# Performance work log

Measured on AMD Instinct MI355X. Metric: run time of the kernel, lower is better.

The kernel has to match this reference:

```python
import jax, jax.numpy as jnp
import numpy as np

EPS_BN = 1e-5
EPS_NORM = 1e-12
USER_NUM, ITEM_NUM = 100000, 50000
N_NODES = USER_NUM + ITEM_NUM
N_EDGES = 2400000
OUT_DIM, HID_DIM = 64, 128
BATCH = 4096


def setup_inputs() -> dict:
    key = jax.random.key(0)
    ks = jax.random.split(key, 12)
    f32 = jnp.float32
    return {
        "user_emb": jax.random.normal(ks[0], (USER_NUM, OUT_DIM), f32) * 0.1,
        "item_emb": jax.random.normal(ks[1], (ITEM_NUM, OUT_DIM), f32) * 0.1,
        "W0": jax.random.normal(ks[2], (OUT_DIM, HID_DIM), f32) * (1.0 / np.sqrt(OUT_DIM)),
        "b0": jnp.zeros((HID_DIM,), f32),
        "g0": jnp.ones((HID_DIM,), f32),
        "beta0": jnp.zeros((HID_DIM,), f32),
        "W1": jax.random.normal(ks[3], (HID_DIM, HID_DIM), f32) * (1.0 / np.sqrt(HID_DIM)),
        "b1": jnp.zeros((HID_DIM,), f32),
        "g1": jnp.ones((HID_DIM,), f32),
        "beta1": jnp.zeros((HID_DIM,), f32),
        "W2": jax.random.normal(ks[4], (HID_DIM, OUT_DIM), f32) * (1.0 / np.sqrt(HID_DIM)),
        "b2": jnp.zeros((OUT_DIM,), f32),
        "user_id": jax.random.randint(ks[5], (BATCH,), 0, USER_NUM),
        "pos_item": jax.random.randint(ks[6], (BATCH,), 0, ITEM_NUM),
        "neg_item": jax.random.randint(ks[7], (BATCH,), 0, ITEM_NUM),
        "edge_index": jax.random.randint(ks[8], (2, N_EDGES), 0, N_NODES),
    }


def _gcn_conv(x, W, b, src, dst, dis):
    # GCNConv with self-loops and symmetric normalization:
    # out_i = sum_{j->i} d_j^{-1/2} d_i^{-1/2} (x_j W) + d_i^{-1} (x_i W) + b
    h = x @ W                                   # [N, F]
    norm = dis[src] * dis[dst]                  # [E]
    msgs = h[src] * norm[:, None]               # [E, F] (irregular gather)
    agg = jax.ops.segment_sum(msgs, dst, num_segments=x.shape[0])
    self_loop = h * (dis * dis)[:, None]        # contribution of added self-loops
    return agg + self_loop + b


def _bn_train(x, gamma, beta):
    mean = jnp.mean(x, axis=0)
    var = jnp.mean((x - mean) ** 2, axis=0)     # biased var, as torch BN uses
    return (x - mean) * jax.lax.rsqrt(var + EPS_BN) * gamma + beta


def _l2norm(x):
    n = jnp.sqrt(jnp.sum(x * x, axis=-1, keepdims=True))
    return x / jnp.maximum(n, EPS_NORM)


def reference(user_emb, item_emb, W0, b0, g0, beta0, W1, b1, g1, beta1, W2, b2,
              user_id, pos_item, neg_item, edge_index):
    N = user_emb.shape[0] + item_emb.shape[0]
    src, dst = edge_index[0], edge_index[1]
    # degree includes self loop (weight 1 per edge + 1 self loop)
    deg = 1.0 + jax.ops.segment_sum(jnp.ones_like(src, user_emb.dtype), dst, num_segments=N)
    dis = jax.lax.rsqrt(deg)

    x = jnp.concatenate([user_emb, item_emb], axis=0)          # [N, OUT_DIM]

    # layer 0: conv -> BN -> ReLU -> (dropout: eval/identity) -> L2-normalize
    x = _l2norm(jax.nn.relu(_bn_train(_gcn_conv(x, W0, b0, src, dst, dis), g0, beta0)))
    # layer 1
    x = _l2norm(jax.nn.relu(_bn_train(_gcn_conv(x, W1, b1, src, dst, dis), g1, beta1)))
    # final conv
    x = _gcn_conv(x, W2, b2, src, dst, dis)                    # [N, OUT_DIM]

    user_embeddings = x[:user_emb.shape[0]]
    item_embeddings = x[user_emb.shape[0]:]
    u = user_embeddings[user_id]
    p = item_embeddings[pos_item]
    n = item_embeddings[neg_item]
    pos_score = jnp.sum(u * p, axis=-1)
    neg_score = jnp.sum(u * n, axis=-1)
    rec_loss = -jnp.mean(jax.nn.log_sigmoid(pos_score - neg_score))
    return rec_loss, x
```

## Files before the change

kernel.cpp:

```cpp
#include <hip/hip_runtime.h>
#include <hip/hip_bf16.h>
#include <math.h>

#define USER_NUM 100000
#define ITEM_NUM 50000
#define N_NODES  150000
#define N_EDGES  2400000
#define OUT_DIM  64
#define HID_DIM  128
#define BATCH    4096
#define EPS_BN   1e-5f

typedef unsigned short ushort_t;
typedef unsigned int uint_t;

__device__ __forceinline__ ushort_t f2bf(float f) {
    uint_t u = __float_as_uint(f);
    u += 0x7FFFu + ((u >> 16) & 1u);
    return (ushort_t)(u >> 16);
}
__device__ __forceinline__ float bf2f(ushort_t s) {
    return __uint_as_float((uint_t)s << 16);
}


__global__ __launch_bounds__(256) void zero_int_kernel(int* __restrict__ p, int n) {
    int i = blockIdx.x * 256 + threadIdx.x;
    if (i < n) p[i] = 0;
}

__global__ __launch_bounds__(256) void count_kernel(const int* __restrict__ dst, int* __restrict__ cnt) {
    int i = blockIdx.x * 256 + threadIdx.x;
    if (i < N_EDGES) atomicAdd(&cnt[dst[i]], 1);
}

__global__ __launch_bounds__(256) void dis_kernel(const int* __restrict__ cnt, float* __restrict__ dis) {
    int i = blockIdx.x * 256 + threadIdx.x;
    if (i < N_NODES) dis[i] = rsqrtf(1.0f + (float)cnt[i]);
}

#define SC_ELEM 1024
#define SC_NB   ((N_NODES + SC_ELEM - 1) / SC_ELEM)

__global__ __launch_bounds__(256) void scan_part_kernel(const int* __restrict__ cnt,
                                                        int* __restrict__ psum) {
    __shared__ int red[4];
    int tid = threadIdx.x;
    int base = blockIdx.x * SC_ELEM + tid * 4;
    int s = 0;
#pragma unroll
    for (int j = 0; j < 4; j++) { int i = base + j; if (i < N_NODES) s += cnt[i]; }
#pragma unroll
    for (int d = 1; d < 64; d <<= 1) s += __shfl_xor(s, d);
    if ((tid & 63) == 0) red[tid >> 6] = s;
    __syncthreads();
    if (tid == 0) psum[blockIdx.x] = red[0] + red[1] + red[2] + red[3];
}

__global__ __launch_bounds__(256) void scan_mid_kernel(int* __restrict__ psum,
                                                       int* __restrict__ off, int nb) {
    __shared__ int lds[256];
    int tid = threadIdx.x;
    int v = (tid < nb) ? psum[tid] : 0;
    lds[tid] = v;
    __syncthreads();
    for (int d = 1; d < 256; d <<= 1) {
        int t = (tid >= d) ? lds[tid - d] : 0;
        __syncthreads();
        lds[tid] += t;
        __syncthreads();
    }
    if (tid < nb) psum[tid] = lds[tid] - v;
    if (tid == 0) off[N_NODES] = lds[255];
}

__global__ __launch_bounds__(256) void scan_emit_kernel(const int* __restrict__ cnt,
                                                        const int* __restrict__ psum,
                                                        int* __restrict__ off,
                                                        int* __restrict__ cur) {
    __shared__ int lds[256];
    int tid = threadIdx.x;
    int base = blockIdx.x * SC_ELEM + tid * 4;
    int v[4]; int s = 0;
#pragma unroll
    for (int j = 0; j < 4; j++) {
        int i = base + j;
        v[j] = (i < N_NODES) ? cnt[i] : 0;
        s += v[j];
    }
    lds[tid] = s;
    __syncthreads();
    for (int d = 1; d < 256; d <<= 1) {
        int t = (tid >= d) ? lds[tid - d] : 0;
        __syncthreads();
        lds[tid] += t;
        __syncthreads();
    }
    int run = psum[blockIdx.x] + lds[tid] - s;
#pragma unroll
    for (int j = 0; j < 4; j++) {
        int i = base + j;
        if (i < N_NODES) { off[i] = run; cur[i] = run; }
        run += v[j];
    }
}

__global__ __launch_bounds__(256) void fill_kernel(const int* __restrict__ src, const int* __restrict__ dst,
                                                   const float* __restrict__ dis,
                                                   int* __restrict__ cursor,
                                                   uint2* __restrict__ csr8) {
    int i = blockIdx.x * 256 + threadIdx.x;
    if (i < N_EDGES) {
        int s = src[i];
        int d = dst[i];
        int p = atomicAdd(&cursor[d], 1);
        uint2 e;
        e.x = (uint_t)s;
        e.y = __float_as_uint(dis[s] * dis[d]);
        csr8[p] = e;
    }
}


__device__ __forceinline__ float4 load4(const float* p) { return *(const float4*)p; }
__device__ __forceinline__ float4 load4(const ushort_t* p) {
    ushort4 u = *(const ushort4*)p;
    return make_float4(bf2f(u.x), bf2f(u.y), bf2f(u.z), bf2f(u.w));
}

template<typename XT, int DIN, int DOUT, int MBLK>
__global__ __launch_bounds__(256) void gemm_kernel(const XT* __restrict__ xlo,
                                                   const XT* __restrict__ xhi, int split,
                                                   const float* __restrict__ W,
                                                   ushort_t* __restrict__ out, int nrows) {
    constexpr int KC    = 32;
    constexpr int NC    = DIN / KC;
    constexpr int XS_PT = MBLK / 32;
    constexpr int WS_PT = DOUT / 32;
    constexpr int NCOLG = DOUT / 8;

    __shared__ float xs[MBLK][KC + 1];
    __shared__ float ws[KC][DOUT];

    const int tid  = threadIdx.x;
    const int row0 = blockIdx.x * MBLK;
    const int colg = tid % NCOLG;
    const int rowg = tid / NCOLG;

    float4 xr[XS_PT], wr[WS_PT];

    auto load_chunk = [&](int kc) {
#pragma unroll
        for (int i = 0; i < XS_PT; i++) {
            int idx = i * 256 + tid;
            int m = idx >> 3, kq = idx & 7;
            int row = row0 + m; if (row > nrows - 1) row = nrows - 1;
            const XT* rp = (row < split) ? xlo + (size_t)row * DIN
                                         : xhi + (size_t)(row - split) * DIN;
            xr[i] = load4(rp + kc + kq * 4);
        }
#pragma unroll
        for (int i = 0; i < WS_PT; i++) {
            int idx = i * 256 + tid;
            int n4 = idx % (DOUT / 4), kk = idx / (DOUT / 4);
            wr[i] = *(const float4*)(W + (size_t)(kc + kk) * DOUT + n4 * 4);
        }
    };
    auto write_chunk = [&]() {
#pragma unroll
        for (int i = 0; i < XS_PT; i++) {
            int idx = i * 256 + tid;
            int m = idx >> 3, kq = idx & 7;
            xs[m][kq * 4 + 0] = xr[i].x;
            xs[m][kq * 4 + 1] = xr[i].y;
            xs[m][kq * 4 + 2] = xr[i].z;
            xs[m][kq * 4 + 3] = xr[i].w;
        }
#pragma unroll
        for (int i = 0; i < WS_PT; i++) {
            int idx = i * 256 + tid;
            int n4 = idx % (DOUT / 4), kk = idx / (DOUT / 4);
            *(float4*)&ws[kk][n4 * 4] = wr[i];
        }
    };

    float acc[8][8];
#pragma unroll
    for (int r = 0; r < 8; r++)
#pragma unroll
        for (int c = 0; c < 8; c++) acc[r][c] = 0.f;

    load_chunk(0);
    write_chunk();
    __syncthreads();

    for (int c = 0; c < NC; c++) {
        if (c + 1 < NC) load_chunk((c + 1) * KC);
#pragma unroll 4
        for (int k = 0; k < KC; k++) {
            float4 wa = *(const float4*)&ws[k][colg * 8];
            float4 wb = *(const float4*)&ws[k][colg * 8 + 4];
            float xv[8];
#pragma unroll
            for (int r = 0; r < 8; r++) xv[r] = xs[rowg * 8 + r][k];
#pragma unroll
            for (int r = 0; r < 8; r++) {
                acc[r][0] = fmaf(xv[r], wa.x, acc[r][0]);
                acc[r][1] = fmaf(xv[r], wa.y, acc[r][1]);
                acc[r][2] = fmaf(xv[r], wa.z, acc[r][2]);
                acc[r][3] = fmaf(xv[r], wa.w, acc[r][3]);
                acc[r][4] = fmaf(xv[r], wb.x, acc[r][4]);
                acc[r][5] = fmaf(xv[r], wb.y, acc[r][5]);
                acc[r][6] = fmaf(xv[r], wb.z, acc[r][6]);
                acc[r][7] = fmaf(xv[r], wb.w, acc[r][7]);
            }
        }
        __syncthreads();
        if (c + 1 < NC) { write_chunk(); __syncthreads(); }
    }

#pragma unroll
    for (int r = 0; r < 8; r++) {
        int row = row0 + rowg * 8 + r;
        if (row < nrows) {
            uint4 pk;
            pk.x = (uint_t)f2bf(acc[r][0]) | ((uint_t)f2bf(acc[r][1]) << 16);
            pk.y = (uint_t)f2bf(acc[r][2]) | ((uint_t)f2bf(acc[r][3]) << 16);
            pk.z = (uint_t)f2bf(acc[r][4]) | ((uint_t)f2bf(acc[r][5]) << 16);
            pk.w = (uint_t)f2bf(acc[r][6]) | ((uint_t)f2bf(acc[r][7]) << 16);
            *(uint4*)&out[(size_t)row * DOUT + colg * 8] = pk;
        }
    }
}


template<int DOUT>
__global__ __launch_bounds__(256) void agg_kernel(const ushort_t* __restrict__ h,
                                                  const float* __restrict__ dis,
                                                  const int* __restrict__ off,
                                                  const uint2* __restrict__ csr8,
                                                  const float* __restrict__ bias,
                                                  float* __restrict__ out, int n) {
    int wave = threadIdx.x >> 6;
    int lane = threadIdx.x & 63;
    int node = blockIdx.x * 4 + wave;
    if (node >= n) return;
    float di  = dis[node];
    int   beg = off[node], end = off[node + 1];
    if (DOUT == 128) {
        const uint_t* hp = (const uint_t*)h;
        float ax = 0.f, ay = 0.f;
        int e = beg;
        for (; e + 4 <= end; e += 4) {
            uint2 e0 = csr8[e], e1 = csr8[e + 1], e2 = csr8[e + 2], e3 = csr8[e + 3];
            uint_t u0 = hp[(size_t)e0.x * 64 + lane];
            uint_t u1 = hp[(size_t)e1.x * 64 + lane];
            uint_t u2 = hp[(size_t)e2.x * 64 + lane];
            uint_t u3 = hp[(size_t)e3.x * 64 + lane];
            float w0 = __uint_as_float(e0.y), w1 = __uint_as_float(e1.y);
            float w2 = __uint_as_float(e2.y), w3 = __uint_as_float(e3.y);
            ax = fmaf(__uint_as_float(u0 << 16), w0, ax);
            ay = fmaf(__uint_as_float(u0 & 0xFFFF0000u), w0, ay);
            ax = fmaf(__uint_as_float(u1 << 16), w1, ax);
            ay = fmaf(__uint_as_float(u1 & 0xFFFF0000u), w1, ay);
            ax = fmaf(__uint_as_float(u2 << 16), w2, ax);
            ay = fmaf(__uint_as_float(u2 & 0xFFFF0000u), w2, ay);
            ax = fmaf(__uint_as_float(u3 << 16), w3, ax);
            ay = fmaf(__uint_as_float(u3 & 0xFFFF0000u), w3, ay);
        }
        for (; e < end; e++) {
            uint2 ev = csr8[e];
            float wv = __uint_as_float(ev.y);
            uint_t u = hp[(size_t)ev.x * 64 + lane];
            ax = fmaf(__uint_as_float(u << 16), wv, ax);
            ay = fmaf(__uint_as_float(u & 0xFFFF0000u), wv, ay);
        }
        uint_t us = hp[(size_t)node * 64 + lane];
        float2 bb = ((const float2*)bias)[lane];
        float dd = di * di;
        float2 o;
        o.x = ax + __uint_as_float(us << 16) * dd + bb.x;
        o.y = ay + __uint_as_float(us & 0xFFFF0000u) * dd + bb.y;
        ((float2*)out)[(size_t)node * 64 + lane] = o;
    } else {
        float ax = 0.f;
        int e = beg;
        for (; e + 4 <= end; e += 4) {
            uint2 e0 = csr8[e], e1 = csr8[e + 1], e2 = csr8[e + 2], e3 = csr8[e + 3];
            float h0 = bf2f(h[(size_t)e0.x * 64 + lane]);
            float h1 = bf2f(h[(size_t)e1.x * 64 + lane]);
            float h2 = bf2f(h[(size_t)e2.x * 64 + lane]);
            float h3 = bf2f(h[(size_t)e3.x * 64 + lane]);
            ax = fmaf(h0, __uint_as_float(e0.y), ax);
            ax = fmaf(h1, __uint_as_float(e1.y), ax);
            ax = fmaf(h2, __uint_as_float(e2.y), ax);
            ax = fmaf(h3, __uint_as_float(e3.y), ax);
        }
        for (; e < end; e++) {
            uint2 ev = csr8[e];
            ax = fmaf(bf2f(h[(size_t)ev.x * 64 + lane]), __uint_as_float(ev.y), ax);
        }
        float hs = bf2f(h[(size_t)node * 64 + lane]);
        out[(size_t)node * 64 + lane] = ax + hs * di * di + bias[lane];
    }
}


#define STATS_NB 512

__global__ __launch_bounds__(128) void stats1_kernel(const float* __restrict__ x,
                                                     double* __restrict__ part) {
    int col = threadIdx.x;
    double a = 0.0, b = 0.0;
    for (int row = blockIdx.x; row < N_NODES; row += STATS_NB) {
        float v = x[(size_t)row * HID_DIM + col];
        a += v;
        b += (double)v * (double)v;
    }
    part[(size_t)blockIdx.x * 256 + col]       = a;
    part[(size_t)blockIdx.x * 256 + 128 + col] = b;
}

__global__ __launch_bounds__(256) void stats2_kernel(const double* __restrict__ part,
                                                     const float* __restrict__ g,
                                                     const float* __restrict__ beta,
                                                     float* __restrict__ a_out,
                                                     float* __restrict__ b_out) {
    __shared__ double red1[4], red2[4];
    int col = blockIdx.x;
    int tid = threadIdx.x;
    double s1 = 0.0, s2 = 0.0;
    for (int p = tid; p < STATS_NB; p += 256) {
        s1 += part[(size_t)p * 256 + col];
        s2 += part[(size_t)p * 256 + 128 + col];
    }
#pragma unroll
    for (int d = 32; d >= 1; d >>= 1) {
        s1 += __shfl_xor(s1, d);
        s2 += __shfl_xor(s2, d);
    }
    int wave = tid >> 6, lane = tid & 63;
    if (lane == 0) { red1[wave] = s1; red2[wave] = s2; }
    __syncthreads();
    if (tid == 0) {
        double t1 = red1[0] + red1[1] + red1[2] + red1[3];
        double t2 = red2[0] + red2[1] + red2[2] + red2[3];
        double mean = t1 / (double)N_NODES;
        double var  = t2 / (double)N_NODES - mean * mean;
        float inv = rsqrtf((float)var + EPS_BN);
        float aa  = g[col] * inv;
        a_out[col] = aa;
        b_out[col] = beta[col] - (float)mean * aa;
    }
}


__global__ __launch_bounds__(256) void bn_relu_l2_kernel(const float* __restrict__ in,
                                                         const float* __restrict__ a,
                                                         const float* __restrict__ b,
                                                         uint_t* __restrict__ outp, int n) {
    int wave = threadIdx.x >> 6;
    int lane = threadIdx.x & 63;
    int row  = blockIdx.x * 4 + wave;
    if (row >= n) return;
    float2 v  = *(const float2*)(in + (size_t)row * 128 + lane * 2);
    float2 aa = *(const float2*)(a + lane * 2);
    float2 bb = *(const float2*)(b + lane * 2);
    float y0 = fmaxf(fmaf(v.x, aa.x, bb.x), 0.f);
    float y1 = fmaxf(fmaf(v.y, aa.y, bb.y), 0.f);
    float ss = y0 * y0 + y1 * y1;
#pragma unroll
    for (int d = 32; d >= 1; d >>= 1) ss += __shfl_xor(ss, d);
    float nn  = sqrtf(ss);
    float inv = 1.f / fmaxf(nn, 1e-12f);
    uint_t pk = (uint_t)f2bf(y0 * inv) | ((uint_t)f2bf(y1 * inv) << 16);
    outp[(size_t)row * 64 + lane] = pk;
}


__global__ void zero_float_kernel(float* p) { *p = 0.f; }

__global__ __launch_bounds__(256) void loss_kernel(const float* __restrict__ X,
                                                   const int* __restrict__ uid,
                                                   const int* __restrict__ pid,
                                                   const int* __restrict__ nid,
                                                   float* __restrict__ out0) {
    int wave = threadIdx.x >> 6;
    int lane = threadIdx.x & 63;
    int b = blockIdx.x * 4 + wave;
    if (b >= BATCH) return;
    const float* u = X + (size_t)uid[b] * OUT_DIM;
    const float* p = X + (size_t)(USER_NUM + pid[b]) * OUT_DIM;
    const float* q = X + (size_t)(USER_NUM + nid[b]) * OUT_DIM;
    float uv = u[lane];
    float ps = uv * p[lane];
    float ns = uv * q[lane];
#pragma unroll
    for (int d = 32; d >= 1; d >>= 1) {
        ps += __shfl_xor(ps, d);
        ns += __shfl_xor(ns, d);
    }
    if (lane == 0) {
        float t  = ns - ps;
        float sp = fmaxf(t, 0.f) + log1pf(expf(-fabsf(t)));
        atomicAdd(out0, sp * (1.0f / BATCH));
    }
}


extern "C" void kernel_launch(void* const* d_in, const int* in_sizes, int n_in,
                              void* d_out, int out_size, void* d_ws, size_t ws_size,
                              hipStream_t stream) {
    const float* user_emb = (const float*)d_in[0];
    const float* item_emb = (const float*)d_in[1];
    const float* W0  = (const float*)d_in[2];
    const float* b0  = (const float*)d_in[3];
    const float* g0  = (const float*)d_in[4];
    const float* be0 = (const float*)d_in[5];
    const float* W1  = (const float*)d_in[6];
    const float* b1  = (const float*)d_in[7];
    const float* g1  = (const float*)d_in[8];
    const float* be1 = (const float*)d_in[9];
    const float* W2  = (const float*)d_in[10];
    const float* b2  = (const float*)d_in[11];
    const int* user_id  = (const int*)d_in[12];
    const int* pos_item = (const int*)d_in[13];
    const int* neg_item = (const int*)d_in[14];
    const int* edge     = (const int*)d_in[15];
    const int* src = edge;
    const int* dst = edge + N_EDGES;

    char* w = (char*)d_ws;
    auto alloc = [&](size_t bytes) -> char* {
        char* r = w;
        w += (bytes + 255) / 256 * 256;
        return r;
    };
    int*      cnt  = (int*)alloc((size_t)N_NODES * 4);
    int*      off  = (int*)alloc((size_t)(N_NODES + 1) * 4);
    int*      cur  = (int*)alloc((size_t)N_NODES * 4);
    uint2*    csr8 = (uint2*)alloc((size_t)N_EDGES * 8);
    float*    dis  = (float*)alloc((size_t)N_NODES * 4);
    int*      psum = (int*)alloc((size_t)SC_NB * 4);
    double*   part = (double*)alloc((size_t)STATS_NB * 256 * 8);
    float*    bn_a = (float*)alloc(128 * 4);
    float*    bn_b = (float*)alloc(128 * 4);
    ushort_t* hbuf = (ushort_t*)alloc((size_t)N_NODES * HID_DIM * 2);
    float*    xbuf = (float*)alloc((size_t)N_NODES * HID_DIM * 4);
    ushort_t* xbf  = (ushort_t*)alloc((size_t)N_NODES * HID_DIM * 2);

    float* out = (float*)d_out;
    float* X   = out + 1;

    const int EB = (N_EDGES + 255) / 256;
    const int NB = (N_NODES + 255) / 256;
    const int AGGB = (N_NODES + 3) / 4;

    zero_int_kernel<<<NB, 256, 0, stream>>>(cnt, N_NODES);
    count_kernel<<<EB, 256, 0, stream>>>(dst, cnt);
    dis_kernel<<<NB, 256, 0, stream>>>(cnt, dis);
    scan_part_kernel<<<SC_NB, 256, 0, stream>>>(cnt, psum);
    scan_mid_kernel<<<1, 256, 0, stream>>>(psum, off, SC_NB);
    scan_emit_kernel<<<SC_NB, 256, 0, stream>>>(cnt, psum, off, cur);
    fill_kernel<<<EB, 256, 0, stream>>>(src, dst, dis, cur, csr8);

    gemm_kernel<float, 64, 128, 128><<<(N_NODES + 127) / 128, 256, 0, stream>>>(
        user_emb, item_emb, USER_NUM, W0, hbuf, N_NODES);
    agg_kernel<128><<<AGGB, 256, 0, stream>>>(hbuf, dis, off, csr8, b0, xbuf, N_NODES);
    stats1_kernel<<<STATS_NB, 128, 0, stream>>>(xbuf, part);
    stats2_kernel<<<128, 256, 0, stream>>>(part, g0, be0, bn_a, bn_b);
    bn_relu_l2_kernel<<<AGGB, 256, 0, stream>>>(xbuf, bn_a, bn_b, (uint_t*)xbf, N_NODES);

    gemm_kernel<ushort_t, 128, 128, 128><<<(N_NODES + 127) / 128, 256, 0, stream>>>(
        xbf, xbf, N_NODES, W1, hbuf, N_NODES);
    agg_kernel<128><<<AGGB, 256, 0, stream>>>(hbuf, dis, off, csr8, b1, xbuf, N_NODES);
    stats1_kernel<<<STATS_NB, 128, 0, stream>>>(xbuf, part);
    stats2_kernel<<<128, 256, 0, stream>>>(part, g1, be1, bn_a, bn_b);
    bn_relu_l2_kernel<<<AGGB, 256, 0, stream>>>(xbuf, bn_a, bn_b, (uint_t*)xbf, N_NODES);

    gemm_kernel<ushort_t, 128, 64, 256><<<(N_NODES + 255) / 256, 256, 0, stream>>>(
        xbf, xbf, N_NODES, W2, hbuf, N_NODES);
    agg_kernel<64><<<AGGB, 256, 0, stream>>>(hbuf, dis, off, csr8, b2, X, N_NODES);

    zero_float_kernel<<<1, 1, 0, stream>>>(out);
    loss_kernel<<<(BATCH + 3) / 4, 256, 0, stream>>>(X, user_id, pos_item, neg_item, out);
}
```

Before: 1.134 ms.

## Build CSR with two-pass bucketed scatter instead of global atomic fill

```diff
diff --git a/kernel.cpp b/kernel.cpp
--- a/kernel.cpp
+++ b/kernel.cpp
@@ -76,8 +76,7 @@
 
 __global__ __launch_bounds__(256) void scan_emit_kernel(const int* __restrict__ cnt,
                                                         const int* __restrict__ psum,
-                                                        int* __restrict__ off,
-                                                        int* __restrict__ cur) {
+                                                        int* __restrict__ off) {
     __shared__ int lds[256];
     int tid = threadIdx.x;
     int base = blockIdx.x * SC_ELEM + tid * 4;
@@ -100,24 +99,66 @@
 #pragma unroll
     for (int j = 0; j < 4; j++) {
         int i = base + j;
-        if (i < N_NODES) { off[i] = run; cur[i] = run; }
+        if (i < N_NODES) off[i] = run;
         run += v[j];
     }
 }
 
-__global__ __launch_bounds__(256) void fill_kernel(const int* __restrict__ src, const int* __restrict__ dst,
-                                                   const float* __restrict__ dis,
-                                                   int* __restrict__ cursor,
-                                                   uint2* __restrict__ csr8) {
-    int i = blockIdx.x * 256 + threadIdx.x;
-    if (i < N_EDGES) {
-        int s = src[i];
+
+#define BSH   9
+#define NBUCK ((N_NODES + 511) / 512)
+#define P1_BLOCKS 512
+
+__global__ __launch_bounds__(256) void bucket_part_kernel(const int* __restrict__ src,
+                                                          const int* __restrict__ dst,
+                                                          const int* __restrict__ off,
+                                                          int* __restrict__ bcur,
+                                                          uint2* __restrict__ temp) {
+    __shared__ int hist[NBUCK];
+    __shared__ int base[NBUCK];
+    const int per = (N_EDGES + P1_BLOCKS - 1) / P1_BLOCKS;
+    const int lo = blockIdx.x * per;
+    int hi = lo + per; if (hi > N_EDGES) hi = N_EDGES;
+    const int tid = threadIdx.x;
+    for (int j = tid; j < NBUCK; j += 256) hist[j] = 0;
+    __syncthreads();
+    for (int i = lo + tid; i < hi; i += 256)
+        atomicAdd(&hist[dst[i] >> BSH], 1);
+    __syncthreads();
+    for (int b = tid; b < NBUCK; b += 256) {
+        int h = hist[b];
+        if (h > 0) base[b] = off[b << BSH] + atomicAdd(&bcur[b], h);
+    }
+    __syncthreads();
+    for (int i = lo + tid; i < hi; i += 256) {
         int d = dst[i];
-        int p = atomicAdd(&cursor[d], 1);
-        uint2 e;
-        e.x = (uint_t)s;
-        e.y = __float_as_uint(dis[s] * dis[d]);
-        csr8[p] = e;
+        int p = atomicAdd(&base[d >> BSH], 1);
+        temp[p] = make_uint2((uint_t)src[i], (uint_t)d);
+    }
+}
+
+__global__ __launch_bounds__(256) void bucket_fine_kernel(const int* __restrict__ off,
+                                                          const float* __restrict__ dis,
+                                                          const uint2* __restrict__ temp,
+                                                          uint2* __restrict__ csr8) {
+    __shared__ int   offs[513];
+    __shared__ int   cur[512];
+    __shared__ float disd[512];
+    const int b  = blockIdx.x;
+    const int lo = b << BSH;
+    int hi = lo + 512; if (hi > N_NODES) hi = N_NODES;
+    const int nn = hi - lo;
+    const int tid = threadIdx.x;
+    for (int j = tid; j <= nn; j += 256) offs[j] = off[lo + j];
+    for (int j = tid; j < nn; j += 256) { cur[j] = 0; disd[j] = dis[lo + j]; }
+    __syncthreads();
+    const int e0 = offs[0], e1 = offs[nn];
+    for (int i = e0 + tid; i < e1; i += 256) {
+        uint2 t = temp[i];
+        int dl = (int)t.y - lo;
+        int p = offs[dl] + atomicAdd(&cur[dl], 1);
+        float wv = dis[t.x] * disd[dl];
+        csr8[p] = make_uint2(t.x, __float_as_uint(wv));
     }
 }
 
@@ -438,7 +479,7 @@
     };
     int*      cnt  = (int*)alloc((size_t)N_NODES * 4);
     int*      off  = (int*)alloc((size_t)(N_NODES + 1) * 4);
-    int*      cur  = (int*)alloc((size_t)N_NODES * 4);
+    int*      bcur = (int*)alloc((size_t)NBUCK * 4);
     uint2*    csr8 = (uint2*)alloc((size_t)N_EDGES * 8);
     float*    dis  = (float*)alloc((size_t)N_NODES * 4);
     int*      psum = (int*)alloc((size_t)SC_NB * 4);
@@ -449,6 +490,8 @@
     float*    xbuf = (float*)alloc((size_t)N_NODES * HID_DIM * 4);
     ushort_t* xbf  = (ushort_t*)alloc((size_t)N_NODES * HID_DIM * 2);
 
+    uint2* temp = (uint2*)hbuf;
+
     float* out = (float*)d_out;
     float* X   = out + 1;
 
@@ -461,8 +504,10 @@
     dis_kernel<<<NB, 256, 0, stream>>>(cnt, dis);
     scan_part_kernel<<<SC_NB, 256, 0, stream>>>(cnt, psum);
     scan_mid_kernel<<<1, 256, 0, stream>>>(psum, off, SC_NB);
-    scan_emit_kernel<<<SC_NB, 256, 0, stream>>>(cnt, psum, off, cur);
-    fill_kernel<<<EB, 256, 0, stream>>>(src, dst, dis, cur, csr8);
+    scan_emit_kernel<<<SC_NB, 256, 0, stream>>>(cnt, psum, off);
+    zero_int_kernel<<<(NBUCK + 255) / 256, 256, 0, stream>>>(bcur, NBUCK);
+    bucket_part_kernel<<<P1_BLOCKS, 256, 0, stream>>>(src, dst, off, bcur, temp);
+    bucket_fine_kernel<<<NBUCK, 256, 0, stream>>>(off, dis, temp, csr8);
 
     gemm_kernel<float, 64, 128, 128><<<(N_NODES + 127) / 128, 256, 0, stream>>>(
         user_emb, item_emb, USER_NUM, W0, hbuf, N_NODES);
```

Result: faster. 1.077 ms (-5.0%).
